# Kernel tuning notes

Measured on AMD Instinct MI355X. Metric: run time of the kernel, lower is better.

The kernel has to match this reference:

```python
import jax, jax.numpy as jnp
import numpy as np

B, K, H, W = 8, 16, 224, 224
RADIUS = 5
WIN = 2 * (RADIUS - 1) + 1  # 9


def setup_inputs() -> dict:
    key = jax.random.key(0)
    k1, k2 = jax.random.split(key)
    # soft segmentation (softmax output in W-Net): positive, rows ~ sum to 1
    logits = jax.random.normal(k1, (B, K, H, W), dtype=jnp.float32)
    seg = jax.nn.softmax(logits, axis=1)
    pad = RADIUS - 1
    padded_seg = jnp.pad(seg, ((0, 0), (0, 0), (pad, pad), (pad, pad)))
    # per-pixel Gaussian-affinity-like weights over the (2r-1)^2 window
    weight = jax.random.uniform(k2, (B, 1, H, W, WIN, WIN), dtype=jnp.float32)
    sum_weight = weight.sum((-1, -2))  # [B,1,H,W], degree d(i)
    return {
        "seg": seg,
        "padded_seg": padded_seg,
        "weight": weight,
        "sum_weight": sum_weight,
        "radius": RADIUS,
        "ncut_k": K,
    }


def reference(seg, padded_seg, weight, sum_weight, radius, ncut_k):
    # seg: [B,K,H,W]; padded_seg: [B,K,H+2(r-1),W+2(r-1)]
    b, k, h, w = seg.shape
    win = 2 * (radius - 1) + 1
    # Fused sliding-window multiply-accumulate: equivalent to
    # cropped_seg.mul(weight).sum(-1).sum(-1) without materializing
    acc = jnp.zeros_like(seg)
    for m in range(win):
        for n in range(win):
            acc = acc + padded_seg[:, :, m:m + h, n:n + w] * weight[:, :, :, :, m, n]
    assocA = (acc * seg).reshape(b, k, -1).sum(-1)        # [B,K]
    assocV = (sum_weight * seg).reshape(b, k, -1).sum(-1)  # [B,K]
    assoc = (assocA / assocV).sum(-1)                      # [B]
    return ncut_k - assoc
```

## Files before the change

### kernel.cpp

```cpp
#include <hip/hip_runtime.h>

#define B 8
#define K 16
#define H 224
#define W 224
#define PH 232
#define PW 232
#define WIN 9
#define NP (B * H * W)

typedef float vf4 __attribute__((ext_vector_type(4), aligned(4)));
typedef float vf4a __attribute__((ext_vector_type(4)));

#define PSTR 708
#define RSTR 44

__global__ __launch_bounds__(256, 3) void ncuts_dw(
    const float* __restrict__ seg,
    const float* __restrict__ padded,
    const float* __restrict__ weight,
    const float* __restrict__ sumw,
    float* __restrict__ ws)
{
    __shared__ float pad_lds[16 * PSTR];
    __shared__ float red[4][16][2];

    const int tid = threadIdx.x;
    const int bid = blockIdx.x;
    const int b   = bid & 7;
    const int rest = bid >> 3;
    const int ht  = rest / 7;
    const int wt  = rest - ht * 7;
    const int h0 = ht * 8, w0 = wt * 32;

#pragma unroll
    for (int i = 0; i < 10; ++i) {
        const int f   = tid + 256 * i;
        const int k   = f / 160;
        const int rem = f - k * 160;
        const int r   = rem / 10;
        const int c   = rem - r * 10;
        vf4a v = *(const vf4a*)(padded +
            (((long)(b * K + k) * PH + (h0 + r)) * PW + (w0 + 4 * c)));
        *(vf4a*)&pad_lds[k * PSTR + r * RSTR + 4 * c] = v;
    }
    __syncthreads();

    const int lane = tid & 63;
    const int q    = lane & 7;
    const int kg   = (lane >> 3) & 3;
    const int rr   = tid >> 5;
    const int h    = h0 + rr;
    const long pix0 = (long)(b * H + h) * W + w0 + 4 * q;
    const float* wbase = weight + pix0 * 81;

    float acc[4][4];
#pragma unroll
    for (int kk = 0; kk < 4; ++kk)
#pragma unroll
        for (int p = 0; p < 4; ++p) acc[kk][p] = 0.f;

#pragma unroll 1
    for (int prl = 0; prl < 9; ++prl) {
        float winK[4][12];
#pragma unroll
        for (int kk = 0; kk < 4; ++kk) {
            const float* lb = &pad_lds[(kg * 4 + kk) * PSTR + (rr + prl) * RSTR + 4 * q];
            vf4a a0 = *(const vf4a*)(lb);
            vf4a a1 = *(const vf4a*)(lb + 4);
            vf4a a2 = *(const vf4a*)(lb + 8);
#pragma unroll
            for (int p = 0; p < 4; ++p) {
                winK[kk][p]     = ((const float*)&a0)[p];
                winK[kk][p + 4] = ((const float*)&a1)[p];
                winK[kk][p + 8] = ((const float*)&a2)[p];
            }
        }
        float wt_[4][9];
#pragma unroll
        for (int p = 0; p < 4; ++p) {
            const float* wp_ = wbase + (long)p * 81 + prl * 9;
            vf4 wa = *(const vf4*)wp_;
            vf4 wb = *(const vf4*)(wp_ + 4);
            const float w8 = wp_[8];
            wt_[p][0] = wa.x; wt_[p][1] = wa.y; wt_[p][2] = wa.z; wt_[p][3] = wa.w;
            wt_[p][4] = wb.x; wt_[p][5] = wb.y; wt_[p][6] = wb.z; wt_[p][7] = wb.w;
            wt_[p][8] = w8;
        }
#pragma unroll
        for (int n = 0; n < 9; ++n)
#pragma unroll
            for (int kk = 0; kk < 4; ++kk)
#pragma unroll
                for (int p = 0; p < 4; ++p)
                    acc[kk][p] = fmaf(winK[kk][p + n], wt_[p][n], acc[kk][p]);
    }

    float aA[4], aV[4];
    {
        const vf4a sw4 = __builtin_nontemporal_load((const vf4a*)(sumw + pix0));
#pragma unroll
        for (int kk = 0; kk < 4; ++kk) {
            const int k = kg * 4 + kk;
            const float* sp = seg + ((long)(b * K + k) * H + h) * W + w0 + 4 * q;
            const vf4a s4 = __builtin_nontemporal_load((const vf4a*)sp);
            float a = 0.f, v = 0.f;
#pragma unroll
            for (int p = 0; p < 4; ++p) {
                a = fmaf(acc[kk][p], ((const float*)&s4)[p], a);
                v = fmaf(((const float*)&sw4)[p], ((const float*)&s4)[p], v);
            }
            aA[kk] = a; aV[kk] = v;
        }
    }
#pragma unroll
    for (int off = 0; off < 4; ++off) {
        const int d = (off < 3) ? (1 << off) : 32;
#pragma unroll
        for (int kk = 0; kk < 4; ++kk) {
            aA[kk] += __shfl_xor(aA[kk], d);
            aV[kk] += __shfl_xor(aV[kk], d);
        }
    }
    const int wv = tid >> 6;
    if ((lane & 39) == 0) {
#pragma unroll
        for (int kk = 0; kk < 4; ++kk) {
            red[wv][kg * 4 + kk][0] = aA[kk];
            red[wv][kg * 4 + kk][1] = aV[kk];
        }
    }
    __syncthreads();
    if (tid < 32) {
        const int k  = tid >> 1;
        const int ab = tid & 1;
        const float v = red[0][k][ab] + red[1][k][ab] + red[2][k][ab] + red[3][k][ab];
        atomicAdd(&ws[ab * 128 + b * 16 + k], v);
    }
}

__global__ void ncuts_final(const float* __restrict__ ws,
                            const int* __restrict__ ncut_k,
                            float* __restrict__ out)
{
    const int t = threadIdx.x;
    const int b = t >> 4;
    const int k = t & 15;
    float r = ws[b * K + k] / ws[128 + b * K + k];
#pragma unroll
    for (int off = 1; off < 16; off <<= 1) r += __shfl_xor(r, off, 16);
    if (k == 0) out[b] = (float)(*ncut_k) - r;
}

extern "C" void kernel_launch(void* const* d_in, const int* in_sizes, int n_in,
                              void* d_out, int out_size, void* d_ws, size_t ws_size,
                              hipStream_t stream) {
    (void)in_sizes; (void)n_in; (void)out_size; (void)ws_size;
    const float* seg    = (const float*)d_in[0];
    const float* padded = (const float*)d_in[1];
    const float* weight = (const float*)d_in[2];
    const float* sumw   = (const float*)d_in[3];
    const int*   nk     = (const int*)d_in[5];
    float* ws  = (float*)d_ws;
    float* out = (float*)d_out;

    hipMemsetAsync(ws, 0, 2 * B * K * sizeof(float), stream);
    ncuts_dw<<<8 * 28 * 7, 256, 0, stream>>>(seg, padded, weight, sumw, ws);
    ncuts_final<<<1, 128, 0, stream>>>(ws, nk, out);
}
```

Baseline: 261.7 us.

## Double-buffer weight row loads with aligned vector loads and full unroll

The window-row loop is fully unrolled and the per-pixel weights for the next row are prefetched into a second register buffer while the current row is consumed. A sched_barrier keeps the compiler from moving the loads. Weight loads become 16-byte-aligned vector loads (three per pixel) with a compile-time rotation to pick elements, replacing the two unaligned vf4 loads plus one scalar load. The prefetch is meant to hide global-memory latency, but the extra 96 registers of weight buffers may push register use past the 3-waves launch bound and cause spills. The aligned loads also fetch some redundant bytes.

```diff
diff --git a/kernel.cpp b/kernel.cpp
--- a/kernel.cpp
+++ b/kernel.cpp
@@ -14,6 +14,45 @@
 
 #define PSTR 708
 #define RSTR 44
+
+#define LOADW(dst, m_) do {                                                  \
+    _Pragma("unroll")                                                        \
+    for (int p = 0; p < 4; ++p) {                                            \
+        const int off = 81 * p + 9 * (m_);                                   \
+        const int fb  = off & ~3;                                            \
+        dst[3*p+0] = *(const vf4a*)(wb + fb);                                \
+        dst[3*p+1] = *(const vf4a*)(wb + fb + 4);                            \
+        dst[3*p+2] = *(const vf4a*)(wb + fb + 8);                            \
+    }                                                                        \
+} while (0)
+
+#define CONS(src, m_) do {                                                   \
+    _Pragma("unroll")                                                        \
+    for (int kk = 0; kk < 4; ++kk) {                                         \
+        const float* lb = &pad_lds[(kg*4+kk)*PSTR + (rr+(m_))*RSTR + 4*q];   \
+        vf4a a0 = *(const vf4a*)lb;                                          \
+        vf4a a1 = *(const vf4a*)(lb + 4);                                    \
+        vf4a a2 = *(const vf4a*)(lb + 8);                                    \
+        float wk[12];                                                        \
+        _Pragma("unroll")                                                    \
+        for (int p2 = 0; p2 < 4; ++p2) {                                     \
+            wk[p2]     = ((const float*)&a0)[p2];                            \
+            wk[p2 + 4] = ((const float*)&a1)[p2];                            \
+            wk[p2 + 8] = ((const float*)&a2)[p2];                            \
+        }                                                                    \
+        _Pragma("unroll")                                                    \
+        for (int p = 0; p < 4; ++p) {                                        \
+            const int rot = (81 * p + 9 * (m_)) & 3;                         \
+            _Pragma("unroll")                                                \
+            for (int n = 0; n < 9; ++n) {                                    \
+                const int ci = rot + n;                                      \
+                acc[kk][p] = fmaf(wk[p + n],                                 \
+                    ((const float*)&src[3*p + (ci >> 2)])[ci & 3],           \
+                    acc[kk][p]);                                             \
+            }                                                                \
+        }                                                                    \
+    }                                                                        \
+} while (0)
 
 __global__ __launch_bounds__(256, 3) void ncuts_dw(
     const float* __restrict__ seg,
@@ -52,7 +91,7 @@
     const int rr   = tid >> 5;
     const int h    = h0 + rr;
     const long pix0 = (long)(b * H + h) * W + w0 + 4 * q;
-    const float* wbase = weight + pix0 * 81;
+    const float* wb = weight + pix0 * 81;
 
     float acc[4][4];
 #pragma unroll
@@ -60,40 +99,17 @@
 #pragma unroll
         for (int p = 0; p < 4; ++p) acc[kk][p] = 0.f;
 
-#pragma unroll 1
-    for (int prl = 0; prl < 9; ++prl) {
-        float winK[4][12];
+    vf4a wA[12], wB[12];
+    LOADW(wA, 0);
 #pragma unroll
-        for (int kk = 0; kk < 4; ++kk) {
-            const float* lb = &pad_lds[(kg * 4 + kk) * PSTR + (rr + prl) * RSTR + 4 * q];
-            vf4a a0 = *(const vf4a*)(lb);
-            vf4a a1 = *(const vf4a*)(lb + 4);
-            vf4a a2 = *(const vf4a*)(lb + 8);
-#pragma unroll
-            for (int p = 0; p < 4; ++p) {
-                winK[kk][p]     = ((const float*)&a0)[p];
-                winK[kk][p + 4] = ((const float*)&a1)[p];
-                winK[kk][p + 8] = ((const float*)&a2)[p];
-            }
+    for (int m = 0; m < 9; ++m) {
+        if (m < 8) {
+            if (m & 1) LOADW(wA, m + 1);
+            else       LOADW(wB, m + 1);
         }
-        float wt_[4][9];
-#pragma unroll
-        for (int p = 0; p < 4; ++p) {
-            const float* wp_ = wbase + (long)p * 81 + prl * 9;
-            vf4 wa = *(const vf4*)wp_;
-            vf4 wb = *(const vf4*)(wp_ + 4);
-            const float w8 = wp_[8];
-            wt_[p][0] = wa.x; wt_[p][1] = wa.y; wt_[p][2] = wa.z; wt_[p][3] = wa.w;
-            wt_[p][4] = wb.x; wt_[p][5] = wb.y; wt_[p][6] = wb.z; wt_[p][7] = wb.w;
-            wt_[p][8] = w8;
-        }
-#pragma unroll
-        for (int n = 0; n < 9; ++n)
-#pragma unroll
-            for (int kk = 0; kk < 4; ++kk)
-#pragma unroll
-                for (int p = 0; p < 4; ++p)
-                    acc[kk][p] = fmaf(winK[kk][p + n], wt_[p][n], acc[kk][p]);
+        __builtin_amdgcn_sched_barrier(0);
+        if (m & 1) CONS(wB, m);
+        else       CONS(wA, m);
     }
 
     float aA[4], aV[4];
```

Measured after the change: 265.8 us. No clear change (+1.6%).

## Stage weights via async global-to-LDS triple buffer, read padded seg directly

Applied to the files above, without the earlier changes.

Stops staging padded_seg in LDS and reads window rows directly from global/cache instead. Streams the per-pixel weight rows into a triple-buffered LDS ring with global_load_lds, using aligned 16-byte chunks with rotation offsets and a swizzle. The aim is coalesced weight loads overlapped with compute, and higher occupancy (launch bound 3→4) from the smaller LDS footprint. The cost is a barrier per window row and uncoalesced, possibly redundant global reads of the padded input.

```diff
diff --git a/kernel.cpp b/kernel.cpp
--- a/kernel.cpp
+++ b/kernel.cpp
@@ -9,20 +9,19 @@
 #define WIN 9
 #define NP (B * H * W)
 
-typedef float vf4 __attribute__((ext_vector_type(4), aligned(4)));
 typedef float vf4a __attribute__((ext_vector_type(4)));
+typedef const __attribute__((address_space(1))) char gchar;
+typedef __attribute__((address_space(3))) char lchar;
 
-#define PSTR 708
-#define RSTR 44
 
-__global__ __launch_bounds__(256, 3) void ncuts_dw(
+__global__ __launch_bounds__(256, 4) void ncuts_dw(
     const float* __restrict__ seg,
     const float* __restrict__ padded,
     const float* __restrict__ weight,
     const float* __restrict__ sumw,
     float* __restrict__ ws)
 {
-    __shared__ float pad_lds[16 * PSTR];
+    __shared__ float wlds[3][3][256][4];
     __shared__ float red[4][16][2];
 
     const int tid = threadIdx.x;
@@ -33,26 +32,25 @@
     const int wt  = rest - ht * 7;
     const int h0 = ht * 8, w0 = wt * 32;
 
-#pragma unroll
-    for (int i = 0; i < 10; ++i) {
-        const int f   = tid + 256 * i;
-        const int k   = f / 160;
-        const int rem = f - k * 160;
-        const int r   = rem / 10;
-        const int c   = rem - r * 10;
-        vf4a v = *(const vf4a*)(padded +
-            (((long)(b * K + k) * PH + (h0 + r)) * PW + (w0 + 4 * c)));
-        *(vf4a*)&pad_lds[k * PSTR + r * RSTR + 4 * c] = v;
-    }
-    __syncthreads();
+    const int pi = tid ^ ((tid >> 3) & 3);
+    const int rs = pi >> 5;
+    const int cs = pi & 31;
+    const long Pg = (long)(b * H + h0 + rs) * W + w0 + cs;
+    const float* wgb = weight + 81 * Pg;
 
     const int lane = tid & 63;
     const int q    = lane & 7;
     const int kg   = (lane >> 3) & 3;
     const int rr   = tid >> 5;
+    const int xq   = (q >> 1) & 3;
     const int h    = h0 + rr;
     const long pix0 = (long)(b * H + h) * W + w0 + 4 * q;
-    const float* wbase = weight + pix0 * 81;
+
+    const float* pb[4];
+#pragma unroll
+    for (int kk = 0; kk < 4; ++kk)
+        pb[kk] = padded + ((long)(b * K + kg * 4 + kk) * PH + (h0 + rr)) * PW
+                 + w0 + 4 * q;
 
     float acc[4][4];
 #pragma unroll
@@ -60,40 +58,62 @@
 #pragma unroll
         for (int p = 0; p < 4; ++p) acc[kk][p] = 0.f;
 
-#pragma unroll 1
-    for (int prl = 0; prl < 9; ++prl) {
-        float winK[4][12];
+    {
+        const int offf = -(cs & 3);
+        const gchar* g0 = (const gchar*)(wgb + offf);
+        lchar* l0 = (lchar*)&wlds[0][0][tid & 192][0];
+        __builtin_amdgcn_global_load_lds(g0,      l0,        16, 0, 0);
+        __builtin_amdgcn_global_load_lds(g0 + 16, l0 + 4096, 16, 0, 0);
+        __builtin_amdgcn_global_load_lds(g0 + 32, l0 + 8192, 16, 0, 0);
+    }
+
+#pragma unroll
+    for (int m = 0; m < 9; ++m) {
+        const int buf = m % 3;
+        __syncthreads();
+        if (m < 8) {
+            const int nb = (m + 1) % 3;
+            const int offf = 9 * (m + 1) - ((cs + m + 1) & 3);
+            const gchar* g0 = (const gchar*)(wgb + offf);
+            lchar* l0 = (lchar*)&wlds[nb][0][tid & 192][0];
+            __builtin_amdgcn_global_load_lds(g0,      l0,        16, 0, 0);
+            __builtin_amdgcn_global_load_lds(g0 + 16, l0 + 4096, 16, 0, 0);
+            __builtin_amdgcn_global_load_lds(g0 + 32, l0 + 8192, 16, 0, 0);
+        }
+        float win[4][12];
 #pragma unroll
         for (int kk = 0; kk < 4; ++kk) {
-            const float* lb = &pad_lds[(kg * 4 + kk) * PSTR + (rr + prl) * RSTR + 4 * q];
-            vf4a a0 = *(const vf4a*)(lb);
+            const float* lb = pb[kk] + m * PW;
+            vf4a a0 = *(const vf4a*)lb;
             vf4a a1 = *(const vf4a*)(lb + 4);
             vf4a a2 = *(const vf4a*)(lb + 8);
 #pragma unroll
-            for (int p = 0; p < 4; ++p) {
-                winK[kk][p]     = ((const float*)&a0)[p];
-                winK[kk][p + 4] = ((const float*)&a1)[p];
-                winK[kk][p + 8] = ((const float*)&a2)[p];
+            for (int t = 0; t < 4; ++t) {
+                win[kk][t]     = ((const float*)&a0)[t];
+                win[kk][t + 4] = ((const float*)&a1)[t];
+                win[kk][t + 8] = ((const float*)&a2)[t];
             }
         }
-        float wt_[4][9];
 #pragma unroll
         for (int p = 0; p < 4; ++p) {
-            const float* wp_ = wbase + (long)p * 81 + prl * 9;
-            vf4 wa = *(const vf4*)wp_;
-            vf4 wb = *(const vf4*)(wp_ + 4);
-            const float w8 = wp_[8];
-            wt_[p][0] = wa.x; wt_[p][1] = wa.y; wt_[p][2] = wa.z; wt_[p][3] = wa.w;
-            wt_[p][4] = wb.x; wt_[p][5] = wb.y; wt_[p][6] = wb.z; wt_[p][7] = wb.w;
-            wt_[p][8] = w8;
-        }
+            const int rot = (p + m) & 3;
+            const int sp  = rr * 32 + 4 * q + (p ^ xq);
+            vf4a c0 = *(const vf4a*)&wlds[buf][0][sp][0];
+            vf4a c1 = *(const vf4a*)&wlds[buf][1][sp][0];
+            vf4a c2 = *(const vf4a*)&wlds[buf][2][sp][0];
+            float wk[12];
 #pragma unroll
-        for (int n = 0; n < 9; ++n)
+            for (int t = 0; t < 4; ++t) {
+                wk[t]     = ((const float*)&c0)[t];
+                wk[t + 4] = ((const float*)&c1)[t];
+                wk[t + 8] = ((const float*)&c2)[t];
+            }
 #pragma unroll
             for (int kk = 0; kk < 4; ++kk)
 #pragma unroll
-                for (int p = 0; p < 4; ++p)
-                    acc[kk][p] = fmaf(winK[kk][p + n], wt_[p][n], acc[kk][p]);
+                for (int n = 0; n < 9; ++n)
+                    acc[kk][p] = fmaf(win[kk][p + n], wk[rot + n], acc[kk][p]);
+        }
     }
 
     float aA[4], aV[4];
```

After: 325.5 us. 1.24x slower.

## Stage weights in LDS via direct global-to-LDS loads, read padded seg from global

Applied to the files above, without the earlier changes.

Swaps which operand goes through shared memory. The per-pixel 9x9 weights, the dominant traffic, are now copied with coalesced global_load_lds into LDS. The padded segmentation is read straight from global memory (cache-resident) instead of being staged. The tile shrinks to 4 rows with 2 classes per thread, doubling the block count. Unaligned weight rows are read as aligned vec4 loads with a rotating offset. This targets the strided, poorly coalesced weight reads, at the cost of more redundant global reads of the padded input.

```diff
diff --git a/kernel.cpp b/kernel.cpp
--- a/kernel.cpp
+++ b/kernel.cpp
@@ -6,103 +6,116 @@
 #define W 224
 #define PH 232
 #define PW 232
-#define WIN 9
 #define NP (B * H * W)
 
-typedef float vf4 __attribute__((ext_vector_type(4), aligned(4)));
 typedef float vf4a __attribute__((ext_vector_type(4)));
+typedef const __attribute__((address_space(1))) char gchar;
+typedef __attribute__((address_space(3))) char lchar;
 
-#define PSTR 708
-#define RSTR 44
 
-__global__ __launch_bounds__(256, 3) void ncuts_dw(
+__global__ __launch_bounds__(256, 3) void ncuts_f(
     const float* __restrict__ seg,
     const float* __restrict__ padded,
     const float* __restrict__ weight,
     const float* __restrict__ sumw,
     float* __restrict__ ws)
 {
-    __shared__ float pad_lds[16 * PSTR];
+    __shared__ __align__(16) float wlds[4 * 2592];
     __shared__ float red[4][16][2];
 
     const int tid = threadIdx.x;
     const int bid = blockIdx.x;
-    const int b   = bid & 7;
+    const int b    = bid & 7;
     const int rest = bid >> 3;
-    const int ht  = rest / 7;
-    const int wt  = rest - ht * 7;
-    const int h0 = ht * 8, w0 = wt * 32;
+    const int ht = rest / 7;
+    const int wt = rest - ht * 7;
+    const int h0 = ht * 4, w0 = wt * 32;
 
+    {
+        const int wv64 = tid & 192;
 #pragma unroll
-    for (int i = 0; i < 10; ++i) {
-        const int f   = tid + 256 * i;
-        const int k   = f / 160;
-        const int rem = f - k * 160;
-        const int r   = rem / 10;
-        const int c   = rem - r * 10;
-        vf4a v = *(const vf4a*)(padded +
-            (((long)(b * K + k) * PH + (h0 + r)) * PW + (w0 + 4 * c)));
-        *(vf4a*)&pad_lds[k * PSTR + r * RSTR + 4 * c] = v;
+        for (int ro = 0; ro < 4; ++ro) {
+            const gchar* gsrc = (const gchar*)(weight
+                + 81L * (((long)(b * H + h0 + ro)) * W + w0)) + (long)tid * 16;
+            lchar* ldst = (lchar*)&wlds[ro * 2592] + wv64 * 16;
+            __builtin_amdgcn_global_load_lds(gsrc,        ldst,        16, 0, 0);
+            __builtin_amdgcn_global_load_lds(gsrc + 4096, ldst + 4096, 16, 0, 0);
+            if (tid < 136)
+                __builtin_amdgcn_global_load_lds(gsrc + 8192, ldst + 8192, 16, 0, 0);
+        }
     }
     __syncthreads();
 
     const int lane = tid & 63;
-    const int q    = lane & 7;
-    const int kg   = (lane >> 3) & 3;
-    const int rr   = tid >> 5;
-    const int h    = h0 + rr;
-    const long pix0 = (long)(b * H + h) * W + w0 + 4 * q;
-    const float* wbase = weight + pix0 * 81;
+    const int q  = lane & 7;
+    const int kg = lane >> 3;
+    const int r  = tid >> 6;
+    const int h  = h0 + r;
+    const long pix0 = ((long)(b * H + h)) * W + w0 + 4 * q;
 
-    float acc[4][4];
+    const float* pb0 = padded + (((long)(b * K + kg * 2 + 0)) * PH + h) * PW + w0 + 4 * q;
+    const float* pb1 = padded + (((long)(b * K + kg * 2 + 1)) * PH + h) * PW + w0 + 4 * q;
+    const float* wq  = &wlds[r * 2592 + 324 * q];
+
+    float acc[2][4];
 #pragma unroll
-    for (int kk = 0; kk < 4; ++kk)
+    for (int kk = 0; kk < 2; ++kk)
 #pragma unroll
         for (int p = 0; p < 4; ++p) acc[kk][p] = 0.f;
 
-#pragma unroll 1
-    for (int prl = 0; prl < 9; ++prl) {
-        float winK[4][12];
 #pragma unroll
-        for (int kk = 0; kk < 4; ++kk) {
-            const float* lb = &pad_lds[(kg * 4 + kk) * PSTR + (rr + prl) * RSTR + 4 * q];
-            vf4a a0 = *(const vf4a*)(lb);
-            vf4a a1 = *(const vf4a*)(lb + 4);
-            vf4a a2 = *(const vf4a*)(lb + 8);
+    for (int mm = 0; mm < 9; ++mm) {
+        float k0[12], k1[12];
+        {
+            const float* a = pb0 + mm * PW;
+            vf4a x = *(const vf4a*)a, y = *(const vf4a*)(a + 4), z = *(const vf4a*)(a + 8);
 #pragma unroll
-            for (int p = 0; p < 4; ++p) {
-                winK[kk][p]     = ((const float*)&a0)[p];
-                winK[kk][p + 4] = ((const float*)&a1)[p];
-                winK[kk][p + 8] = ((const float*)&a2)[p];
+            for (int t = 0; t < 4; ++t) {
+                k0[t] = ((const float*)&x)[t];
+                k0[t + 4] = ((const float*)&y)[t];
+                k0[t + 8] = ((const float*)&z)[t];
             }
         }
-        float wt_[4][9];
+        {
+            const float* a = pb1 + mm * PW;
+            vf4a x = *(const vf4a*)a, y = *(const vf4a*)(a + 4), z = *(const vf4a*)(a + 8);
+#pragma unroll
+            for (int t = 0; t < 4; ++t) {
+                k1[t] = ((const float*)&x)[t];
+                k1[t + 4] = ((const float*)&y)[t];
+                k1[t + 8] = ((const float*)&z)[t];
+            }
+        }
+        float ww[4][12];
 #pragma unroll
         for (int p = 0; p < 4; ++p) {
-            const float* wp_ = wbase + (long)p * 81 + prl * 9;
-            vf4 wa = *(const vf4*)wp_;
-            vf4 wb = *(const vf4*)(wp_ + 4);
-            const float w8 = wp_[8];
-            wt_[p][0] = wa.x; wt_[p][1] = wa.y; wt_[p][2] = wa.z; wt_[p][3] = wa.w;
-            wt_[p][4] = wb.x; wt_[p][5] = wb.y; wt_[p][6] = wb.z; wt_[p][7] = wb.w;
-            wt_[p][8] = w8;
+            const int base = 81 * p + 9 * mm - ((p + mm) & 3);
+            vf4a x = *(const vf4a*)(wq + base);
+            vf4a y = *(const vf4a*)(wq + base + 4);
+            vf4a z = *(const vf4a*)(wq + base + 8);
+#pragma unroll
+            for (int t = 0; t < 4; ++t) {
+                ww[p][t] = ((const float*)&x)[t];
+                ww[p][t + 4] = ((const float*)&y)[t];
+                ww[p][t + 8] = ((const float*)&z)[t];
+            }
         }
 #pragma unroll
         for (int n = 0; n < 9; ++n)
 #pragma unroll
-            for (int kk = 0; kk < 4; ++kk)
-#pragma unroll
-                for (int p = 0; p < 4; ++p)
-                    acc[kk][p] = fmaf(winK[kk][p + n], wt_[p][n], acc[kk][p]);
+            for (int p = 0; p < 4; ++p) {
+                acc[0][p] = fmaf(k0[p + n], ww[p][((p + mm) & 3) + n], acc[0][p]);
+                acc[1][p] = fmaf(k1[p + n], ww[p][((p + mm) & 3) + n], acc[1][p]);
+            }
     }
 
-    float aA[4], aV[4];
+    float aA[2], aV[2];
     {
         const vf4a sw4 = __builtin_nontemporal_load((const vf4a*)(sumw + pix0));
 #pragma unroll
-        for (int kk = 0; kk < 4; ++kk) {
-            const int k = kg * 4 + kk;
-            const float* sp = seg + ((long)(b * K + k) * H + h) * W + w0 + 4 * q;
+        for (int kk = 0; kk < 2; ++kk) {
+            const int k = kg * 2 + kk;
+            const float* sp = seg + (((long)(b * K + k)) * H + h) * W + w0 + 4 * q;
             const vf4a s4 = __builtin_nontemporal_load((const vf4a*)sp);
             float a = 0.f, v = 0.f;
 #pragma unroll
@@ -114,20 +127,18 @@
         }
     }
 #pragma unroll
-    for (int off = 0; off < 4; ++off) {
-        const int d = (off < 3) ? (1 << off) : 32;
+    for (int d = 1; d <= 4; d <<= 1) {
 #pragma unroll
-        for (int kk = 0; kk < 4; ++kk) {
+        for (int kk = 0; kk < 2; ++kk) {
             aA[kk] += __shfl_xor(aA[kk], d);
             aV[kk] += __shfl_xor(aV[kk], d);
         }
     }
-    const int wv = tid >> 6;
-    if ((lane & 39) == 0) {
+    if (q == 0) {
 #pragma unroll
-        for (int kk = 0; kk < 4; ++kk) {
-            red[wv][kg * 4 + kk][0] = aA[kk];
-            red[wv][kg * 4 + kk][1] = aV[kk];
+        for (int kk = 0; kk < 2; ++kk) {
+            red[r][kg * 2 + kk][0] = aA[kk];
+            red[r][kg * 2 + kk][1] = aV[kk];
         }
     }
     __syncthreads();
@@ -165,6 +176,6 @@
     float* out = (float*)d_out;
 
     hipMemsetAsync(ws, 0, 2 * B * K * sizeof(float), stream);
-    ncuts_dw<<<8 * 28 * 7, 256, 0, stream>>>(seg, padded, weight, sumw, ws);
+    ncuts_f<<<8 * 56 * 7, 256, 0, stream>>>(seg, padded, weight, sumw, ws);
     ncuts_final<<<1, 128, 0, stream>>>(ws, nk, out);
 }
```

After: 243.7 us. 6.9% less time.
